# Kernel tuning notes

Measured on AMD Instinct MI355X. Metric: run time of the kernel, lower is better.

## Reference

```python
import jax, jax.numpy as jnp
import numpy as np

B, S, V, P = 16, 100, 50000, 45
WE, PE, H = 100, 50, 400
H2 = 2 * H  # bilstm output size


def _lstm(x, Wih, Whh, b):
    """Unidirectional LSTM over time. x: [B,S,D] -> h: [B,S,H]. PyTorch gate order i,f,g,o."""
    Hs = Whh.shape[1]
    def step(carry, xt):
        h, c = carry
        g = xt @ Wih.T + h @ Whh.T + b
        i, f, gg, o = jnp.split(g, 4, axis=-1)
        c = jax.nn.sigmoid(f) * c + jax.nn.sigmoid(i) * jnp.tanh(gg)
        h = jax.nn.sigmoid(o) * jnp.tanh(c)
        return (h, c), h
    Bn = x.shape[0]
    init = (jnp.zeros((Bn, Hs), x.dtype), jnp.zeros((Bn, Hs), x.dtype))
    _, hs = jax.lax.scan(step, init, jnp.swapaxes(x, 0, 1))
    return jnp.swapaxes(hs, 0, 1)


def _bilstm_layer(x, Wf_ih, Wf_hh, bf, Wb_ih, Wb_hh, bb):
    hf = _lstm(x, Wf_ih, Wf_hh, bf)
    hb = _lstm(x[:, ::-1, :], Wb_ih, Wb_hh, bb)[:, ::-1, :]
    return jnp.concatenate([hf, hb], axis=-1)


def setup_inputs() -> dict:
    key = jax.random.key(0)
    ks = jax.random.split(key, 24)
    def n(k, shape, s=0.1):
        return jax.random.normal(k, shape, jnp.float32) * s
    inp = {
        "input_tokens": jax.random.randint(ks[0], (B, S), 0, V),
        "input_pos": jax.random.randint(ks[1], (B, S), 0, P),
        "input_head": jax.random.randint(ks[2], (B, S), 0, S),
        "word_W": n(ks[3], (V, WE)),
        "pos_W": n(ks[4], (P, PE)),
        "l0f_Wih": n(ks[5], (4 * H, WE + PE)), "l0f_Whh": n(ks[6], (4 * H, H)), "l0f_b": n(ks[7], (4 * H,)),
        "l0b_Wih": n(ks[8], (4 * H, WE + PE)), "l0b_Whh": n(ks[9], (4 * H, H)), "l0b_b": n(ks[10], (4 * H,)),
        "l1f_Wih": n(ks[11], (4 * H, H2)), "l1f_Whh": n(ks[12], (4 * H, H)), "l1f_b": n(ks[13], (4 * H,)),
        "l1b_Wih": n(ks[14], (4 * H, H2)), "l1b_Whh": n(ks[15], (4 * H, H)), "l1b_b": n(ks[16], (4 * H,)),
        "ua_W": n(ks[17], (H2, H2)), "ua_b": n(ks[18], (H2,)),
        "wa_W": n(ks[19], (H2, H2)), "wa_b": n(ks[20], (H2,)),
        "va_W": n(ks[21], (H2,)),
    }
    return inp


def reference(input_tokens, input_pos, input_head, word_W, pos_W,
              l0f_Wih, l0f_Whh, l0f_b, l0b_Wih, l0b_Whh, l0b_b,
              l1f_Wih, l1f_Whh, l1f_b, l1b_Wih, l1b_Whh, l1b_b,
              ua_W, ua_b, wa_W, wa_b, va_W):
    # embeddings (dropout is identity at eval)
    x = jnp.concatenate([word_W[input_tokens], pos_W[input_pos]], axis=-1)  # [B,S,150]
    h1 = _bilstm_layer(x, l0f_Wih, l0f_Whh, l0f_b, l0b_Wih, l0b_Whh, l0b_b)   # [B,S,H2]
    out = _bilstm_layer(h1, l1f_Wih, l1f_Whh, l1f_b, l1b_Wih, l1b_Whh, l1b_b)  # [B,S,H2]

    # batched additive biaffine scoring for targets i = 1..S-1 over all source positions j
    ua = out @ ua_W.T + ua_b  # u_a(source)  [B,S,H2]
    wa = out @ wa_W.T + wa_b  # w_a(target)  [B,S,H2]
    # g[b,t,j] = v_a . tanh(ua[b,j] + wa[b,t+1])
    g = jnp.einsum('btjh,h->btj', jnp.tanh(ua[:, None, :, :] + wa[:, 1:, None, :]), va_W)  # [B,S-1,S]
    # mask: output[:, j, 0] == output[:, i, 0]  (masks self, matching torch's output.eq(target)[:,:,0])
    mask = out[:, 1:, 0][:, :, None] == out[:, :, 0][:, None, :]  # [B,S-1,S]
    g = jnp.where(mask, -10000.0, g)
    logp = jax.nn.log_softmax(g, axis=2)  # log_softmax over source positions (torch dim=1)

    # loss: sum over i of NLLLoss(mean over batch, ignore_index=-1)
    gold = input_head[:, 1:]  # [B,S-1]
    valid = (gold != -1)
    nll = -jnp.take_along_axis(logp, jnp.clip(gold, 0, S - 1)[:, :, None], axis=2)[..., 0]
    nll = nll * valid.astype(logp.dtype)
    denom = jnp.maximum(valid.sum(axis=0), 1).astype(logp.dtype)
    loss = jnp.sum(nll.sum(axis=0) / denom)

    parent_prob_table = jnp.exp(logp)  # [B,S-1,S]
    preds = jnp.argmax(parent_prob_table, axis=2)  # [B,S-1]
    return (loss, preds, parent_prob_table)
```

## Files before the change

### kernel.cpp

```cpp
#include <hip/hip_runtime.h>

#define BB 16
#define SS 100
#define HH 400
#define H2 800
#define G4 1600
#define DIN0 150
#define KP0 160

#define OFF_GF   240000ULL
#define OFF_GB   2800000ULL
#define OFF_H1   5360000ULL
#define OFF_OUT2 6640000ULL
#define OFF_NLL  8078400ULL
#define OFF_EXH  8081600ULL
#define EX_U16_PER_PLANE 1331200ULL

typedef _Float16 f16x8 __attribute__((ext_vector_type(8)));
typedef float    f32x4 __attribute__((ext_vector_type(4)));
typedef unsigned long long u64x2 __attribute__((ext_vector_type(2)));

static __device__ __forceinline__ unsigned chkp(unsigned long long q) {
    return ((unsigned)q == 0xFFFFFFFFu) | ((unsigned)(q >> 32) == 0xFFFFFFFFu);
}
static __device__ __forceinline__ unsigned long long sanq(unsigned long long q) {
    if ((unsigned)q == 0xFFFFFFFFu)         q &= 0xFFFFFFFF00000000ull;
    if ((unsigned)(q >> 32) == 0xFFFFFFFFu) q &= 0x00000000FFFFFFFFull;
    return q;
}

static __device__ __forceinline__ void cvt8(const float* v, f16x8& hi, f16x8& lo)
{
#pragma unroll
    for (int i = 0; i < 8; i++) {
        _Float16 h = (_Float16)v[i];
        hi[i] = h;
        lo[i] = (_Float16)((v[i] - (float)h) * 2048.f);
    }
}
static __device__ __forceinline__ void cvt_pair8(float4 a, float4 b,
                                                 f16x8& hi, f16x8& lo)
{
    float v[8] = {a.x, a.y, a.z, a.w, b.x, b.y, b.z, b.w};
    cvt8(v, hi, lo);
}

#define AROW 40

__global__ __launch_bounds__(256) void gemm_l0_embed_dual(
    const int* __restrict__ tok, const int* __restrict__ pos,
    const float* __restrict__ wW, const float* __restrict__ pW,
    const float* __restrict__ W0, const float* __restrict__ b0, float* __restrict__ C0,
    const float* __restrict__ W1, const float* __restrict__ b1, float* __restrict__ C1,
    unsigned int* __restrict__ poison, int poison_words)
{
    {
        int nthreads = gridDim.x * gridDim.y * 256;
        int gtid = (blockIdx.y * gridDim.x + blockIdx.x) * 256 + threadIdx.x;
        for (int i = gtid; i < poison_words; i += nthreads) poison[i] = 0xFFFFFFFFu;
    }

    int half = gridDim.x >> 1;
    int sel = blockIdx.x >= half;
    int bx = blockIdx.x - (sel ? half : 0);
    const float* W = sel ? W1 : W0;
    const float* bias = sel ? b1 : b0;
    float* C = sel ? C1 : C0;

    int tid = threadIdx.x;
    int wv = tid >> 6, l = tid & 63;
    int lm = l & 15, lk = l >> 4;
    int rs = bx * 64 + wv * 16;
    int n0 = blockIdx.y * 64;

    __shared__ __attribute__((aligned(16))) unsigned short AhiS[2][64 * AROW];
    __shared__ __attribute__((aligned(16))) unsigned short AloS[2][64 * AROW];

    int sr = tid >> 2, sc = (tid & 3) * 8;
    int t_ = tok[n0 + sr], p_ = pos[n0 + sr];

    const float* wrow = W + (size_t)(rs + lm) * DIN0;

    f32x4 accH[4], accX[4];
#pragma unroll
    for (int ct = 0; ct < 4; ct++) {
        accH[ct] = {0.f, 0.f, 0.f, 0.f};
        accX[ct] = {0.f, 0.f, 0.f, 0.f};
    }

    float a8[8];
#pragma unroll
    for (int e = 0; e < 8; e++) {
        int k = sc + e;
        a8[e] = (k < 100) ? wW[t_ * 100 + k]
              : (k < DIN0) ? pW[p_ * 50 + (k - 100)] : 0.f;
    }
    float w8[8];
#pragma unroll
    for (int e = 0; e < 8; e++) {
        int k = lk * 8 + e;
        w8[e] = (k < DIN0) ? wrow[k] : 0.f;
    }
    {
        f16x8 h, lo2; cvt8(a8, h, lo2);
        *(f16x8*)&AhiS[0][sr * AROW + sc] = h;
        *(f16x8*)&AloS[0][sr * AROW + sc] = lo2;
    }

    const int nkt = 5;
    for (int kt = 0; kt < nkt; kt++) {
        __syncthreads();
        bool more = (kt + 1 < nkt);
        float a8n[8], w8n[8];
        if (more) {
            int kb = (kt + 1) << 5;
#pragma unroll
            for (int e = 0; e < 8; e++) {
                int k = kb + sc + e;
                a8n[e] = (k < 100) ? wW[t_ * 100 + k]
                       : (k < DIN0) ? pW[p_ * 50 + (k - 100)] : 0.f;
            }
#pragma unroll
            for (int e = 0; e < 8; e++) {
                int k = kb + lk * 8 + e;
                w8n[e] = (k < DIN0) ? wrow[k] : 0.f;
            }
        }
        f16x8 wh, wl; cvt8(w8, wh, wl);
        int buf = kt & 1;
#pragma unroll
        for (int ct = 0; ct < 4; ct++) {
            f16x8 ah = *(const f16x8*)&AhiS[buf][(ct * 16 + lm) * AROW + lk * 8];
            f16x8 al = *(const f16x8*)&AloS[buf][(ct * 16 + lm) * AROW + lk * 8];
            accH[ct] = __builtin_amdgcn_mfma_f32_16x16x32_f16(wh, ah, accH[ct], 0, 0, 0);
            accX[ct] = __builtin_amdgcn_mfma_f32_16x16x32_f16(wh, al, accX[ct], 0, 0, 0);
            accX[ct] = __builtin_amdgcn_mfma_f32_16x16x32_f16(wl, ah, accX[ct], 0, 0, 0);
        }
        if (more) {
            f16x8 h, lo2; cvt8(a8n, h, lo2);
            *(f16x8*)&AhiS[buf ^ 1][sr * AROW + sc] = h;
            *(f16x8*)&AloS[buf ^ 1][sr * AROW + sc] = lo2;
#pragma unroll
            for (int e = 0; e < 8; e++) w8[e] = w8n[e];
        }
    }

    float4 bv = *(const float4*)&bias[rs + lk * 4];
#pragma unroll
    for (int ct = 0; ct < 4; ct++) {
        f32x4 v = accH[ct] + accX[ct] * (1.f / 2048.f);
        float4 o;
        o.x = v[0] + bv.x; o.y = v[1] + bv.y; o.z = v[2] + bv.z; o.w = v[3] + bv.w;
        *(float4*)&C[(size_t)(n0 + ct * 16 + lm) * G4 + rs + lk * 4] = o;
    }
}

__global__ __launch_bounds__(256) void gemm_nt_mfma_dual(
    const float* __restrict__ A,
    const float* __restrict__ W0, const float* __restrict__ b0, float* __restrict__ C0,
    const float* __restrict__ W1, const float* __restrict__ b1, float* __restrict__ C1,
    int K, int R,
    unsigned int* __restrict__ poison, int poison_words)
{
    if (poison) {
        int nthreads = gridDim.x * gridDim.y * 256;
        int gtid = (blockIdx.y * gridDim.x + blockIdx.x) * 256 + threadIdx.x;
        for (int i = gtid; i < poison_words; i += nthreads) poison[i] = 0xFFFFFFFFu;
    }

    int half = gridDim.x >> 1;
    int sel = blockIdx.x >= half;
    int bx = blockIdx.x - (sel ? half : 0);
    const float* W = sel ? W1 : W0;
    const float* bias = sel ? b1 : b0;
    float* C = sel ? C1 : C0;

    int tid = threadIdx.x;
    int wv = tid >> 6, l = tid & 63;
    int lm = l & 15, lk = l >> 4;
    int rs = bx * 64 + wv * 16;
    bool active = (rs < R);
    int n0 = blockIdx.y * 64;

    __shared__ __attribute__((aligned(16))) unsigned short AhiS[2][64 * AROW];
    __shared__ __attribute__((aligned(16))) unsigned short AloS[2][64 * AROW];

    int sr = tid >> 2, sc = (tid & 3) * 8;
    const float* arow_g = A + (size_t)(n0 + sr) * K + sc;
    const float* wrow = W + (size_t)((active ? rs : 0) + lm) * K + lk * 8;

    f32x4 accH[4], accX[4];
#pragma unroll
    for (int ct = 0; ct < 4; ct++) {
        accH[ct] = {0.f, 0.f, 0.f, 0.f};
        accX[ct] = {0.f, 0.f, 0.f, 0.f};
    }

    float a8[8];
    *(float4*)a8       = *(const float4*)arow_g;
    *(float4*)(a8 + 4) = *(const float4*)(arow_g + 4);
    float4 wA = {0,0,0,0}, wB = {0,0,0,0};
    if (active) { wA = *(const float4*)wrow; wB = *(const float4*)(wrow + 4); }
    {
        f16x8 h, lo2; cvt8(a8, h, lo2);
        *(f16x8*)&AhiS[0][sr * AROW + sc] = h;
        *(f16x8*)&AloS[0][sr * AROW + sc] = lo2;
    }

    int nkt = K >> 5;
    for (int kt = 0; kt < nkt; kt++) {
        __syncthreads();
        bool more = (kt + 1 < nkt);
        float a8n[8]; float4 wAn = {0,0,0,0}, wBn = {0,0,0,0};
        if (more) {
            int kb = (kt + 1) << 5;
            *(float4*)a8n       = *(const float4*)(arow_g + kb);
            *(float4*)(a8n + 4) = *(const float4*)(arow_g + kb + 4);
            if (active) {
                wAn = *(const float4*)(wrow + kb);
                wBn = *(const float4*)(wrow + kb + 4);
            }
        }
        if (active) {
            f16x8 wh, wl; cvt_pair8(wA, wB, wh, wl);
            int buf = kt & 1;
#pragma unroll
            for (int ct = 0; ct < 4; ct++) {
                f16x8 ah = *(const f16x8*)&AhiS[buf][(ct * 16 + lm) * AROW + lk * 8];
                f16x8 al = *(const f16x8*)&AloS[buf][(ct * 16 + lm) * AROW + lk * 8];
                accH[ct] = __builtin_amdgcn_mfma_f32_16x16x32_f16(wh, ah, accH[ct], 0, 0, 0);
                accX[ct] = __builtin_amdgcn_mfma_f32_16x16x32_f16(wh, al, accX[ct], 0, 0, 0);
                accX[ct] = __builtin_amdgcn_mfma_f32_16x16x32_f16(wl, ah, accX[ct], 0, 0, 0);
            }
        }
        if (more) {
            f16x8 h, lo2; cvt8(a8n, h, lo2);
            *(f16x8*)&AhiS[(kt & 1) ^ 1][sr * AROW + sc] = h;
            *(f16x8*)&AloS[(kt & 1) ^ 1][sr * AROW + sc] = lo2;
            wA = wAn; wB = wBn;
        }
    }

    if (!active) return;
    float4 bv = *(const float4*)&bias[rs + lk * 4];
#pragma unroll
    for (int ct = 0; ct < 4; ct++) {
        f32x4 v = accH[ct] + accX[ct] * (1.f / 2048.f);
        float4 o;
        o.x = v[0] + bv.x; o.y = v[1] + bv.y; o.z = v[2] + bv.z; o.w = v[3] + bv.w;
        *(float4*)&C[(size_t)(n0 + ct * 16 + lm) * R + rs + lk * 4] = o;
    }
}

__global__ __launch_bounds__(64, 1) void lstm_layer_kernel(
    const float* __restrict__ Gf, const float* __restrict__ Gb,
    const float* __restrict__ Wf, const float* __restrict__ Wb,
    float* __restrict__ hbuf,
    unsigned short* __restrict__ exhi,
    unsigned short* __restrict__ exlo)
{
    const int dir = blockIdx.x / 100;
    const int wg  = blockIdx.x % 100;
    const int j0  = wg * 4;
    const float* __restrict__ G = dir ? Gb : Gf;
    const float* __restrict__ W = dir ? Wb : Wf;

    const int l   = threadIdx.x;
    const int b   = l & 15;
    const int hi4 = l >> 4;

    __shared__ __attribute__((aligned(16))) unsigned short ahi[13 * 64 * 8];
    __shared__ __attribute__((aligned(16))) unsigned short alo[13 * 64 * 8];
    __shared__ float gl[16 * 17];

    {
        const int m = b;
        const int g = m >> 2, jj = m & 3;
        const float* wrow = W + (size_t)(g * HH + j0 + jj) * HH;
        for (int kt = 0; kt < 13; kt++) {
            for (int e = 0; e < 8; e++) {
                int k = kt * 32 + hi4 * 8 + e;
                float w = (k < HH) ? wrow[k] : 0.f;
                _Float16 wh = (_Float16)w;
                _Float16 wl = (_Float16)((w - (float)wh) * 2048.f);
                ahi[(kt * 64 + l) * 8 + e] = __builtin_bit_cast(unsigned short, wh);
                alo[(kt * 64 + l) * 8 + e] = __builtin_bit_cast(unsigned short, wl);
            }
        }
    }
    __syncthreads();

    float c_reg = 0.f;
    unsigned short* exh_d = exhi + (size_t)dir * 100 * 13 * 512;
    unsigned short* exl_d = exlo + (size_t)dir * 100 * 13 * 512;
    const int pad_lane = (hi4 >= 2);

    for (int s = 0; s < SS; s++) {
        const int time = dir ? (SS - 1 - s) : s;
        f32x4 gpre = *(const f32x4*)&G[(size_t)(b * SS + time) * G4 + hi4 * HH + j0];

        f32x4 acc;
        if (s > 0) {
            const unsigned long long* pbh =
                (const unsigned long long*)(exh_d + (size_t)(s - 1) * 13 * 512);
            const unsigned long long* pbl =
                (const unsigned long long*)(exl_d + (size_t)(s - 1) * 13 * 512);
            u64x2 vh2[13], vl2[13];
            vh2[12] = {0ull, 0ull};
            vl2[12] = {0ull, 0ull};
            unsigned bad = 1;
            for (int guard = 0; guard < (1 << 13); guard++) {
                bad = 0;
#pragma unroll
                for (int kt = 0; kt < 12; kt++) {
                    size_t q = (size_t)(kt * 64 + l) * 2;
                    vh2[kt][0] = __hip_atomic_load(pbh + q,     __ATOMIC_RELAXED, __HIP_MEMORY_SCOPE_AGENT);
                    vh2[kt][1] = __hip_atomic_load(pbh + q + 1, __ATOMIC_RELAXED, __HIP_MEMORY_SCOPE_AGENT);
                    vl2[kt][0] = __hip_atomic_load(pbl + q,     __ATOMIC_RELAXED, __HIP_MEMORY_SCOPE_AGENT);
                    vl2[kt][1] = __hip_atomic_load(pbl + q + 1, __ATOMIC_RELAXED, __HIP_MEMORY_SCOPE_AGENT);
                }
                if (!pad_lane) {
                    size_t q = (size_t)(12 * 64 + l) * 2;
                    vh2[12][0] = __hip_atomic_load(pbh + q,     __ATOMIC_RELAXED, __HIP_MEMORY_SCOPE_AGENT);
                    vh2[12][1] = __hip_atomic_load(pbh + q + 1, __ATOMIC_RELAXED, __HIP_MEMORY_SCOPE_AGENT);
                    vl2[12][0] = __hip_atomic_load(pbl + q,     __ATOMIC_RELAXED, __HIP_MEMORY_SCOPE_AGENT);
                    vl2[12][1] = __hip_atomic_load(pbl + q + 1, __ATOMIC_RELAXED, __HIP_MEMORY_SCOPE_AGENT);
                    bad |= chkp(vh2[12][0]) | chkp(vh2[12][1])
                         | chkp(vl2[12][0]) | chkp(vl2[12][1]);
                }
#pragma unroll
                for (int kt = 0; kt < 12; kt++) {
                    bad |= chkp(vh2[kt][0]) | chkp(vh2[kt][1])
                         | chkp(vl2[kt][0]) | chkp(vl2[kt][1]);
                }
                if (__ballot(bad != 0) == 0ull) break;
                __builtin_amdgcn_s_sleep(2);
            }
            if (bad) {
#pragma unroll
                for (int kt = 0; kt < 13; kt++) {
                    vh2[kt][0] = sanq(vh2[kt][0]); vh2[kt][1] = sanq(vh2[kt][1]);
                    vl2[kt][0] = sanq(vl2[kt][0]); vl2[kt][1] = sanq(vl2[kt][1]);
                }
            }
            asm volatile("" ::: "memory");

            f32x4 aHH = gpre;
            f32x4 aHL = {0.f, 0.f, 0.f, 0.f};
            f32x4 aLH = {0.f, 0.f, 0.f, 0.f};
#pragma unroll
            for (int kt = 0; kt < 13; kt++) {
                f16x8 bhv = __builtin_bit_cast(f16x8, vh2[kt]);
                f16x8 blv = __builtin_bit_cast(f16x8, vl2[kt]);
                f16x8 wh = *(const f16x8*)&ahi[(kt * 64 + l) * 8];
                f16x8 wl = *(const f16x8*)&alo[(kt * 64 + l) * 8];
                aHH = __builtin_amdgcn_mfma_f32_16x16x32_f16(wh, bhv, aHH, 0, 0, 0);
                aHL = __builtin_amdgcn_mfma_f32_16x16x32_f16(wh, blv, aHL, 0, 0, 0);
                aLH = __builtin_amdgcn_mfma_f32_16x16x32_f16(wl, bhv, aLH, 0, 0, 0);
            }
            acc = aHH + (aHL + aLH) * (1.f / 2048.f);
        } else {
            acc = gpre;
        }

#pragma unroll
        for (int q = 0; q < 4; q++) gl[(4 * hi4 + q) * 17 + b] = acc[q];
        __syncthreads();

        const int jj = hi4;
        float gi = gl[( 0 + jj) * 17 + b];
        float gf = gl[( 4 + jj) * 17 + b];
        float gg = gl[( 8 + jj) * 17 + b];
        float go = gl[(12 + jj) * 17 + b];
        __syncthreads();

        float si = 1.f / (1.f + expf(-gi));
        float sf = 1.f / (1.f + expf(-gf));
        float tg = tanhf(gg);
        float so = 1.f / (1.f + expf(-go));
        float c  = sf * c_reg + si * tg;
        c_reg = c;
        float h  = so * tanhf(c);

        if (s < SS - 1) {
            _Float16 hh = (_Float16)h;
            _Float16 hl = (_Float16)((h - (float)hh) * 2048.f);
            unsigned uh = __builtin_bit_cast(unsigned short, hh);
            unsigned ul = __builtin_bit_cast(unsigned short, hl);
            unsigned ph = uh | (((unsigned)__shfl_down((int)uh, 16)) << 16);
            unsigned pl = ul | (((unsigned)__shfl_down((int)ul, 16)) << 16);
            if ((jj & 1) == 0) {
                int k0 = j0 + jj;
                int kt = k0 >> 5, ko = k0 & 31;
                int lg = ko >> 3, e = ko & 7;
                size_t u16idx = ((size_t)(s * 13 + kt) * 64 + (lg * 16 + b)) * 8 + e;
                __hip_atomic_store((unsigned*)(exh_d + u16idx), ph,
                                   __ATOMIC_RELAXED, __HIP_MEMORY_SCOPE_AGENT);
                __hip_atomic_store((unsigned*)(exl_d + u16idx), pl,
                                   __ATOMIC_RELAXED, __HIP_MEMORY_SCOPE_AGENT);
            }
        }

        hbuf[(size_t)(b * SS + time) * H2 + dir * HH + j0 + jj] = h;
    }
}

#define ITILE 11
__global__ __launch_bounds__(256) void attn_scores_softmax_kernel(
    const float* __restrict__ ua, const float* __restrict__ wa,
    const float* __restrict__ va, const float* __restrict__ out2,
    const int* __restrict__ head, float* __restrict__ outb,
    float* __restrict__ nll)
{
    int b  = blockIdx.x / 9;
    int i0 = (blockIdx.x % 9) * ITILE;
    int tid = threadIdx.x;
    __shared__ float ua_t[100][101];
    __shared__ float wa_t[ITILE][102];
    __shared__ float sacc[ITILE][101];
    __shared__ float va_t[100];
    __shared__ float h0[100];

    for (int p = tid; p < ITILE * 101; p += 256) ((float*)sacc)[p] = 0.f;
    if (tid < 100) h0[tid] = out2[(size_t)(b * SS + tid) * H2];

    for (int ht = 0; ht < 8; ht++) {
        int hh0 = ht * 100;
        __syncthreads();
        for (int p = tid; p < 100 * 100; p += 256) {
            int j = p / 100, hh = p % 100;
            ua_t[j][hh] = ua[(size_t)(b * SS + j) * H2 + hh0 + hh];
        }
        for (int p = tid; p < ITILE * 100; p += 256) {
            int il = p / 100, hh = p % 100;
            wa_t[il][hh] = wa[(size_t)(b * SS + i0 + il + 1) * H2 + hh0 + hh];
        }
        if (tid < 100) va_t[tid] = va[hh0 + tid];
        __syncthreads();
        for (int p = tid; p < ITILE * 100; p += 256) {
            int il = p / 100, j = p % 100;
            float acc = 0.f;
#pragma unroll 4
            for (int hh = 0; hh < 100; hh++) {
                float x = ua_t[j][hh] + wa_t[il][hh];
                float z = __expf(2.f * x);
                float th = 1.f - 2.f * __builtin_amdgcn_rcpf(z + 1.f);
                acc = fmaf(th, va_t[hh], acc);
            }
            sacc[il][j] += acc;
        }
    }
    __syncthreads();

    int wv = tid >> 6, ln = tid & 63;
    for (int il = wv; il < ITILE; il += 4) {
        int i = i0 + il;
        int bi = b * 99 + i;
        float h_t = h0[i + 1];
        int j1 = ln, j2 = ln + 64;
        float s1 = sacc[il][j1];
        if (h0[j1] == h_t) s1 = -10000.0f;
        float s2 = -1e30f;
        if (j2 < 100) {
            s2 = sacc[il][j2];
            if (h0[j2] == h_t) s2 = -10000.0f;
        }
        float v = s1; int vi = j1;
        if (s2 > v) { v = s2; vi = j2; }
        for (int k = 32; k >= 1; k >>= 1) {
            float vo = __shfl_xor(v, k);
            int   io = __shfl_xor(vi, k);
            if (vo > v || (vo == v && io < vi)) { v = vo; vi = io; }
        }
        float m = v; int amax = vi;
        float e1 = __expf(s1 - m);
        float e2 = (j2 < 100) ? __expf(s2 - m) : 0.f;
        float sum = e1 + e2;
        for (int k = 32; k >= 1; k >>= 1) sum += __shfl_xor(sum, k);
        float inv = 1.f / sum;
        outb[1 + 1584 + (size_t)bi * 100 + j1] = e1 * inv;
        if (j2 < 100) outb[1 + 1584 + (size_t)bi * 100 + j2] = e2 * inv;
        if (ln == 0) {
            outb[1 + bi] = (float)amax;
            int gold = head[b * SS + i + 1];
            bool valid = (gold != -1);
            int gc = gold < 0 ? 0 : (gold > 99 ? 99 : gold);
            float sgc = sacc[il][gc];
            if (h0[gc] == h_t) sgc = -10000.0f;
            nll[bi] = valid ? -(sgc - m - logf(sum)) : 0.f;
        }
    }
}

__global__ __launch_bounds__(128) void loss_kernel(
    const float* __restrict__ nll, const int* __restrict__ head,
    float* __restrict__ outb)
{
    __shared__ float red[128];
    int tid = threadIdx.x;
    float contrib = 0.f;
    if (tid < 99) {
        int i = tid;
        float tot = 0.f; int cv = 0;
        for (int b = 0; b < BB; b++) {
            tot += nll[b * 99 + i];
            cv += (head[b * SS + i + 1] != -1) ? 1 : 0;
        }
        int denom = cv > 0 ? cv : 1;
        contrib = tot / (float)denom;
    }
    red[tid] = contrib;
    __syncthreads();
    for (int off = 64; off >= 1; off >>= 1) {
        if (tid < off) red[tid] += red[tid + off];
        __syncthreads();
    }
    if (tid == 0) outb[0] = red[0];
}

extern "C" void kernel_launch(void* const* d_in, const int* in_sizes, int n_in,
                              void* d_out, int out_size, void* d_ws, size_t ws_size,
                              hipStream_t stream) {
    const int*   tok     = (const int*)d_in[0];
    const int*   pos     = (const int*)d_in[1];
    const int*   head    = (const int*)d_in[2];
    const float* word_W  = (const float*)d_in[3];
    const float* pos_W   = (const float*)d_in[4];
    const float* l0f_Wih = (const float*)d_in[5];
    const float* l0f_Whh = (const float*)d_in[6];
    const float* l0f_b   = (const float*)d_in[7];
    const float* l0b_Wih = (const float*)d_in[8];
    const float* l0b_Whh = (const float*)d_in[9];
    const float* l0b_b   = (const float*)d_in[10];
    const float* l1f_Wih = (const float*)d_in[11];
    const float* l1f_Whh = (const float*)d_in[12];
    const float* l1f_b   = (const float*)d_in[13];
    const float* l1b_Wih = (const float*)d_in[14];
    const float* l1b_Whh = (const float*)d_in[15];
    const float* l1b_b   = (const float*)d_in[16];
    const float* ua_W    = (const float*)d_in[17];
    const float* ua_b    = (const float*)d_in[18];
    const float* wa_W    = (const float*)d_in[19];
    const float* wa_b    = (const float*)d_in[20];
    const float* va_W    = (const float*)d_in[21];

    float* ws   = (float*)d_ws;
    float* gf   = ws + OFF_GF;
    float* gb   = ws + OFF_GB;
    float* h1   = ws + OFF_H1;
    float* out2 = ws + OFF_OUT2;
    float* nllb = ws + OFF_NLL;
    unsigned short* exhi = (unsigned short*)(ws + OFF_EXH);
    unsigned short* exlo = exhi + EX_U16_PER_PLANE;
    float* outf = (float*)d_out;

    gemm_l0_embed_dual<<<dim3(50, 25), 256, 0, stream>>>(
        tok, pos, word_W, pos_W,
        l0f_Wih, l0f_b, gf, l0b_Wih, l0b_b, gb,
        (unsigned int*)exhi, (int)EX_U16_PER_PLANE);
    lstm_layer_kernel<<<dim3(200), 64, 0, stream>>>(
        gf, gb, l0f_Whh, l0b_Whh, h1, exhi, exlo);
    gemm_nt_mfma_dual<<<dim3(50, 25), 256, 0, stream>>>(
        h1, l1f_Wih, l1f_b, gf, l1b_Wih, l1b_b, gb, H2, G4,
        (unsigned int*)exhi, (int)EX_U16_PER_PLANE);
    lstm_layer_kernel<<<dim3(200), 64, 0, stream>>>(
        gf, gb, l1f_Whh, l1b_Whh, out2, exhi, exlo);
    gemm_nt_mfma_dual<<<dim3(26, 25), 256, 0, stream>>>(
        out2, ua_W, ua_b, gf, wa_W, wa_b, gb, H2, H2, nullptr, 0);
    attn_scores_softmax_kernel<<<dim3(16 * 9), 256, 0, stream>>>(
        gf, gb, va_W, out2, head, outf, nllb);
    loss_kernel<<<dim3(1), 128, 0, stream>>>(nllb, head, outf);
}
```

Measured before the change: 1.276 ms.

## Group four LSTM waves per workgroup and share polled hidden state via LDS

The persistent LSTM kernel now runs 50 workgroups of 256 threads instead of 200 single-wave workgroups. Each wave owns four hidden units, and the four waves split the polling of the previous step's hidden state across k-tiles, staging it in shared memory so each block reads global memory once instead of four times. Readiness is coordinated with per-wave flags and block barriers inside the spin loop. This cuts global polling traffic and the number of agents spinning on cross-block atomics, at the cost of extra barriers per timestep and a wait for the slowest wave.

```diff
diff --git a/kernel.cpp b/kernel.cpp
--- a/kernel.cpp
+++ b/kernel.cpp
@@ -7,6 +7,7 @@
 #define G4 1600
 #define DIN0 150
 #define KP0 160
+#define LWGS 25
 
 #define OFF_GF   240000ULL
 #define OFF_GB   2800000ULL
@@ -18,7 +19,6 @@
 
 typedef _Float16 f16x8 __attribute__((ext_vector_type(8)));
 typedef float    f32x4 __attribute__((ext_vector_type(4)));
-typedef unsigned long long u64x2 __attribute__((ext_vector_type(2)));
 
 static __device__ __forceinline__ unsigned chkp(unsigned long long q) {
     return ((unsigned)q == 0xFFFFFFFFu) | ((unsigned)(q >> 32) == 0xFFFFFFFFu);
@@ -252,30 +252,35 @@
     }
 }
 
-__global__ __launch_bounds__(64, 1) void lstm_layer_kernel(
+__global__ __launch_bounds__(256, 1) void lstm_layer_kernel(
     const float* __restrict__ Gf, const float* __restrict__ Gb,
     const float* __restrict__ Wf, const float* __restrict__ Wb,
     float* __restrict__ hbuf,
     unsigned short* __restrict__ exhi,
     unsigned short* __restrict__ exlo)
 {
-    const int dir = blockIdx.x / 100;
-    const int wg  = blockIdx.x % 100;
-    const int j0  = wg * 4;
+    const int dir = blockIdx.x / LWGS;
+    const int wg  = blockIdx.x % LWGS;
+    const int j0w = wg * 16;
     const float* __restrict__ G = dir ? Gb : Gf;
     const float* __restrict__ W = dir ? Wb : Wf;
 
-    const int l   = threadIdx.x;
+    const int tid = threadIdx.x;
+    const int wv  = tid >> 6;
+    const int l   = tid & 63;
     const int b   = l & 15;
     const int hi4 = l >> 4;
-
-    __shared__ __attribute__((aligned(16))) unsigned short ahi[13 * 64 * 8];
-    __shared__ __attribute__((aligned(16))) unsigned short alo[13 * 64 * 8];
-    __shared__ float gl[16 * 17];
+    const int j0  = j0w + wv * 4;
+
+    __shared__ __attribute__((aligned(16))) unsigned short ahi[4][13 * 64 * 8];
+    __shared__ __attribute__((aligned(16))) unsigned short alo[4][13 * 64 * 8];
+    __shared__ __attribute__((aligned(16))) unsigned short hshhi[13 * 64 * 8];
+    __shared__ __attribute__((aligned(16))) unsigned short hshlo[13 * 64 * 8];
+    __shared__ float gl[4][16 * 17];
+    __shared__ int rdy[4];
 
     {
-        const int m = b;
-        const int g = m >> 2, jj = m & 3;
+        const int g = b >> 2, jj = b & 3;
         const float* wrow = W + (size_t)(g * HH + j0 + jj) * HH;
         for (int kt = 0; kt < 13; kt++) {
             for (int e = 0; e < 8; e++) {
@@ -283,17 +288,24 @@
                 float w = (k < HH) ? wrow[k] : 0.f;
                 _Float16 wh = (_Float16)w;
                 _Float16 wl = (_Float16)((w - (float)wh) * 2048.f);
-                ahi[(kt * 64 + l) * 8 + e] = __builtin_bit_cast(unsigned short, wh);
-                alo[(kt * 64 + l) * 8 + e] = __builtin_bit_cast(unsigned short, wl);
-            }
-        }
-    }
+                ahi[wv][(kt * 64 + l) * 8 + e] = __builtin_bit_cast(unsigned short, wh);
+                alo[wv][(kt * 64 + l) * 8 + e] = __builtin_bit_cast(unsigned short, wl);
+            }
+        }
+    }
+    if (tid < 4) rdy[tid] = 0;
     __syncthreads();
 
+    const int ju = tid >> 4;
+    const int b2 = tid & 15;
     float c_reg = 0.f;
+
+    const int ktA4[4] = {0, 4, 7, 10};
+    const int ktB4[4] = {4, 7, 10, 13};
+    const int ktA = ktA4[wv], ktB = ktB4[wv];
+
     unsigned short* exh_d = exhi + (size_t)dir * 100 * 13 * 512;
     unsigned short* exl_d = exlo + (size_t)dir * 100 * 13 * 512;
-    const int pad_lane = (hi4 >= 2);
 
     for (int s = 0; s < SS; s++) {
         const int time = dir ? (SS - 1 - s) : s;
@@ -305,55 +317,62 @@
                 (const unsigned long long*)(exh_d + (size_t)(s - 1) * 13 * 512);
             const unsigned long long* pbl =
                 (const unsigned long long*)(exl_d + (size_t)(s - 1) * 13 * 512);
-            u64x2 vh2[13], vl2[13];
-            vh2[12] = {0ull, 0ull};
-            vl2[12] = {0ull, 0ull};
-            unsigned bad = 1;
-            for (int guard = 0; guard < (1 << 13); guard++) {
-                bad = 0;
-#pragma unroll
-                for (int kt = 0; kt < 12; kt++) {
-                    size_t q = (size_t)(kt * 64 + l) * 2;
-                    vh2[kt][0] = __hip_atomic_load(pbh + q,     __ATOMIC_RELAXED, __HIP_MEMORY_SCOPE_AGENT);
-                    vh2[kt][1] = __hip_atomic_load(pbh + q + 1, __ATOMIC_RELAXED, __HIP_MEMORY_SCOPE_AGENT);
-                    vl2[kt][0] = __hip_atomic_load(pbl + q,     __ATOMIC_RELAXED, __HIP_MEMORY_SCOPE_AGENT);
-                    vl2[kt][1] = __hip_atomic_load(pbl + q + 1, __ATOMIC_RELAXED, __HIP_MEMORY_SCOPE_AGENT);
+            unsigned long long vh[4][2], vl[4][2];
+            bool mine = false;
+            for (int guard = 0; ; guard++) {
+                if (!mine) {
+                    unsigned bad = 0;
+                    for (int kt = ktA; kt < ktB; kt++) {
+                        int ki = kt - ktA;
+                        if (kt == 12 && hi4 >= 2) {
+                            vh[ki][0] = vh[ki][1] = 0ull;
+                            vl[ki][0] = vl[ki][1] = 0ull;
+                            continue;
+                        }
+                        size_t q = (size_t)(kt * 64 + l) * 2;
+                        vh[ki][0] = __hip_atomic_load(pbh + q,     __ATOMIC_RELAXED, __HIP_MEMORY_SCOPE_AGENT);
+                        vh[ki][1] = __hip_atomic_load(pbh + q + 1, __ATOMIC_RELAXED, __HIP_MEMORY_SCOPE_AGENT);
+                        vl[ki][0] = __hip_atomic_load(pbl + q,     __ATOMIC_RELAXED, __HIP_MEMORY_SCOPE_AGENT);
+                        vl[ki][1] = __hip_atomic_load(pbl + q + 1, __ATOMIC_RELAXED, __HIP_MEMORY_SCOPE_AGENT);
+                        bad |= chkp(vh[ki][0]) | chkp(vh[ki][1])
+                             | chkp(vl[ki][0]) | chkp(vl[ki][1]);
+                    }
+                    bool force = (guard >= (1 << 13));
+                    if ((__ballot(bad != 0) == 0ull) || force) {
+                        for (int kt = ktA; kt < ktB; kt++) {
+                            int ki = kt - ktA;
+                            if (force) {
+                                vh[ki][0] = sanq(vh[ki][0]); vh[ki][1] = sanq(vh[ki][1]);
+                                vl[ki][0] = sanq(vl[ki][0]); vl[ki][1] = sanq(vl[ki][1]);
+                            }
+                            int base = (kt * 64 + l) * 8;
+                            *(unsigned long long*)&hshhi[base]     = vh[ki][0];
+                            *(unsigned long long*)&hshhi[base + 4] = vh[ki][1];
+                            *(unsigned long long*)&hshlo[base]     = vl[ki][0];
+                            *(unsigned long long*)&hshlo[base + 4] = vl[ki][1];
+                        }
+                        mine = true;
+                        if (l == 0) rdy[wv] = 1;
+                    }
                 }
-                if (!pad_lane) {
-                    size_t q = (size_t)(12 * 64 + l) * 2;
-                    vh2[12][0] = __hip_atomic_load(pbh + q,     __ATOMIC_RELAXED, __HIP_MEMORY_SCOPE_AGENT);
-                    vh2[12][1] = __hip_atomic_load(pbh + q + 1, __ATOMIC_RELAXED, __HIP_MEMORY_SCOPE_AGENT);
-                    vl2[12][0] = __hip_atomic_load(pbl + q,     __ATOMIC_RELAXED, __HIP_MEMORY_SCOPE_AGENT);
-                    vl2[12][1] = __hip_atomic_load(pbl + q + 1, __ATOMIC_RELAXED, __HIP_MEMORY_SCOPE_AGENT);
-                    bad |= chkp(vh2[12][0]) | chkp(vh2[12][1])
-                         | chkp(vl2[12][0]) | chkp(vl2[12][1]);
-                }
-#pragma unroll
-                for (int kt = 0; kt < 12; kt++) {
-                    bad |= chkp(vh2[kt][0]) | chkp(vh2[kt][1])
-                         | chkp(vl2[kt][0]) | chkp(vl2[kt][1]);
-                }
-                if (__ballot(bad != 0) == 0ull) break;
-                __builtin_amdgcn_s_sleep(2);
-            }
-            if (bad) {
-#pragma unroll
-                for (int kt = 0; kt < 13; kt++) {
-                    vh2[kt][0] = sanq(vh2[kt][0]); vh2[kt][1] = sanq(vh2[kt][1]);
-                    vl2[kt][0] = sanq(vl2[kt][0]); vl2[kt][1] = sanq(vl2[kt][1]);
-                }
-            }
-            asm volatile("" ::: "memory");
+                __syncthreads();
+                int all = rdy[0] & rdy[1] & rdy[2] & rdy[3];
+                __syncthreads();
+                if (all) break;
+                __builtin_amdgcn_s_sleep(1);
+            }
+            if (tid < 4) rdy[tid] = 0;
 
             f32x4 aHH = gpre;
             f32x4 aHL = {0.f, 0.f, 0.f, 0.f};
             f32x4 aLH = {0.f, 0.f, 0.f, 0.f};
 #pragma unroll
             for (int kt = 0; kt < 13; kt++) {
-                f16x8 bhv = __builtin_bit_cast(f16x8, vh2[kt]);
-                f16x8 blv = __builtin_bit_cast(f16x8, vl2[kt]);
-                f16x8 wh = *(const f16x8*)&ahi[(kt * 64 + l) * 8];
-                f16x8 wl = *(const f16x8*)&alo[(kt * 64 + l) * 8];
+                int base = (kt * 64 + l) * 8;
+                f16x8 bhv = *(const f16x8*)&hshhi[base];
+                f16x8 blv = *(const f16x8*)&hshlo[base];
+                f16x8 wh = *(const f16x8*)&ahi[wv][base];
+                f16x8 wl = *(const f16x8*)&alo[wv][base];
                 aHH = __builtin_amdgcn_mfma_f32_16x16x32_f16(wh, bhv, aHH, 0, 0, 0);
                 aHL = __builtin_amdgcn_mfma_f32_16x16x32_f16(wh, blv, aHL, 0, 0, 0);
                 aLH = __builtin_amdgcn_mfma_f32_16x16x32_f16(wl, bhv, aLH, 0, 0, 0);
@@ -364,14 +383,14 @@
         }
 
 #pragma unroll
-        for (int q = 0; q < 4; q++) gl[(4 * hi4 + q) * 17 + b] = acc[q];
-        __syncthreads();
-
-        const int jj = hi4;
-        float gi = gl[( 0 + jj) * 17 + b];
-        float gf = gl[( 4 + jj) * 17 + b];
-        float gg = gl[( 8 + jj) * 17 + b];
-        float go = gl[(12 + jj) * 17 + b];
+        for (int q = 0; q < 4; q++) gl[wv][(4 * hi4 + q) * 17 + b] = acc[q];
+        __syncthreads();
+
+        const int wq = ju >> 2, jj = ju & 3;
+        float gi = gl[wq][( 0 + jj) * 17 + b2];
+        float gf = gl[wq][( 4 + jj) * 17 + b2];
+        float gg = gl[wq][( 8 + jj) * 17 + b2];
+        float go = gl[wq][(12 + jj) * 17 + b2];
         __syncthreads();
 
         float si = 1.f / (1.f + expf(-gi));
@@ -389,11 +408,11 @@
             unsigned ul = __builtin_bit_cast(unsigned short, hl);
             unsigned ph = uh | (((unsigned)__shfl_down((int)uh, 16)) << 16);
             unsigned pl = ul | (((unsigned)__shfl_down((int)ul, 16)) << 16);
-            if ((jj & 1) == 0) {
-                int k0 = j0 + jj;
+            if ((ju & 1) == 0) {
+                int k0 = j0w + ju;
                 int kt = k0 >> 5, ko = k0 & 31;
                 int lg = ko >> 3, e = ko & 7;
-                size_t u16idx = ((size_t)(s * 13 + kt) * 64 + (lg * 16 + b)) * 8 + e;
+                size_t u16idx = ((size_t)(s * 13 + kt) * 64 + (lg * 16 + b2)) * 8 + e;
                 __hip_atomic_store((unsigned*)(exh_d + u16idx), ph,
                                    __ATOMIC_RELAXED, __HIP_MEMORY_SCOPE_AGENT);
                 __hip_atomic_store((unsigned*)(exl_d + u16idx), pl,
@@ -401,7 +420,7 @@
             }
         }
 
-        hbuf[(size_t)(b * SS + time) * H2 + dir * HH + j0 + jj] = h;
+        hbuf[(size_t)(b2 * SS + time) * H2 + dir * HH + j0w + ju] = h;
     }
 }
 
@@ -558,12 +577,12 @@
         tok, pos, word_W, pos_W,
         l0f_Wih, l0f_b, gf, l0b_Wih, l0b_b, gb,
         (unsigned int*)exhi, (int)EX_U16_PER_PLANE);
-    lstm_layer_kernel<<<dim3(200), 64, 0, stream>>>(
+    lstm_layer_kernel<<<dim3(2 * LWGS), 256, 0, stream>>>(
         gf, gb, l0f_Whh, l0b_Whh, h1, exhi, exlo);
     gemm_nt_mfma_dual<<<dim3(50, 25), 256, 0, stream>>>(
         h1, l1f_Wih, l1f_b, gf, l1b_Wih, l1b_b, gb, H2, G4,
         (unsigned int*)exhi, (int)EX_U16_PER_PLANE);
-    lstm_layer_kernel<<<dim3(200), 64, 0, stream>>>(
+    lstm_layer_kernel<<<dim3(2 * LWGS), 256, 0, stream>>>(
         gf, gb, l1f_Whh, l1b_Whh, out2, exhi, exlo);
     gemm_nt_mfma_dual<<<dim3(26, 25), 256, 0, stream>>>(
         out2, ua_W, ua_b, gf, wa_W, wa_b, gb, H2, H2, nullptr, 0);
```

Result: slower. 1.889 ms (+48.0%).
